# Performance work log

Hardware: AMD Instinct MI355X
Metric: run time of the kernel (lower is better)

## Reference

```python
import jax, jax.numpy as jnp
import numpy as np

B, CI, CO, H, W = 16, 256, 256, 64, 64
WDIM, NUM_FREQ, FREQ_DIM = 512, 16, 512
KS, PAD = 3, 1
SR = 64.0
LR_MULT = 1.0 / SR
GAIN = float(np.sqrt(1.0 / (CI * KS * KS)))
FREQ_GAIN = float(np.sqrt(1.0 / (FREQ_DIM * 2)))


def setup_inputs() -> dict:
    key = jax.random.key(0)
    ks = jax.random.split(key, 7)
    x = jax.random.normal(ks[0], (B, CI, H, W), dtype=jnp.float32)
    temb = jax.random.normal(ks[1], (B, WDIM), dtype=jnp.float32)
    basis = jax.random.normal(ks[2], (CI, KS, KS, FREQ_DIM), dtype=jnp.float32)
    magnitude = jax.random.normal(ks[3], (NUM_FREQ, CI, FREQ_DIM), dtype=jnp.float32)
    out_linear = jax.random.normal(ks[4], (CO, FREQ_DIM), dtype=jnp.float32)
    # FullyConnectedLayer init: weight = randn * (weight_init/lr_mult) = randn (both 1/SR)
    affine_w = jax.random.normal(ks[5], (NUM_FREQ, WDIM), dtype=jnp.float32)
    # bias param stores bias_init / lr_mult = 1 / (1/SR) = SR
    affine_b = jnp.full((NUM_FREQ,), SR, dtype=jnp.float32)
    conv_bias = jnp.zeros((CO,), dtype=jnp.float32)
    return {"x": x, "temb": temb, "basis": basis, "magnitude": magnitude,
            "out_linear": out_linear, "affine_w": affine_w, "affine_b": affine_b,
            "conv_bias": conv_bias}


def reference(x, temb, basis, magnitude, out_linear, affine_w, affine_b, conv_bias):
    # affine (FullyConnectedLayer, linear activation)
    w = affine_w * (LR_MULT / np.sqrt(WDIM))          # weight_gain
    s = temb @ w.T + affine_b * LR_MULT               # [B, K] per-sample freq weights
    # mix magnitude per sample: [K,I,F],[B,K] -> [B,I,F]
    mag_b = jnp.einsum('kif,bk->bif', magnitude, s) / np.sqrt(NUM_FREQ)
    # per-sample dynamic kernels: [I,h,w,F],[B,I,F],[O,F] -> [B,O,I,h,w]
    kernel = jnp.einsum('ihwf,bif,of->boihw', basis, mag_b, out_linear)
    kernel = kernel * (FREQ_GAIN * GAIN)
    kernel = kernel.reshape(B * CO, CI, KS, KS)
    # grouped conv, groups = batch
    xg = x.reshape(1, B * CI, H, W)
    y = jax.lax.conv_general_dilated(
        xg, kernel, window_strides=(1, 1), padding=[(PAD, PAD), (PAD, PAD)],
        dimension_numbers=('NCHW', 'OIHW', 'NCHW'), feature_group_count=B)
    y = y.reshape(B, CO, H, W)
    return jax.nn.silu(y) + conv_bias[None, :, None, None]
```

## Files before the change

kernel.cpp:

```cpp
#include <hip/hip_runtime.h>
#include <hip/hip_bf16.h>
#include <math.h>

#define B_    16
#define CI_   256
#define CO_   256
#define H_    64
#define W_    64
#define WDIM_ 512
#define NF_   16
#define FD_   512

typedef short bf16x8 __attribute__((ext_vector_type(8)));
typedef short s16x8  __attribute__((ext_vector_type(8)));
typedef float f32x4  __attribute__((ext_vector_type(4)));

__device__ __forceinline__ short f2bf(float f) {
  union { float f; unsigned u; } x; x.f = f;
  unsigned r = (x.u + 0x7FFFu + ((x.u >> 16) & 1u)) >> 16;
  return (short)r;
}
__device__ __forceinline__ float bf2f(short s) {
  union { unsigned u; float f; } x; x.u = ((unsigned)(unsigned short)s) << 16;
  return x.f;
}

__device__ __forceinline__ void gload16(const short* g, short* l) {
  __builtin_amdgcn_global_load_lds(
      (const __attribute__((address_space(1))) void*)g,
      (__attribute__((address_space(3))) void*)l, 16, 0, 0);
}

__device__ __forceinline__ size_t koff(int b, int kb, int cc, int t, int o) {
  return ((((((size_t)b * 4 + kb) * 8 + cc) * 9 + t) * 256) + o) * 8;
}
__device__ __forceinline__ size_t xoff(int b, int kb, int cc, int hp, int wp) {
  return ((((((size_t)b * 4 + kb) * 8 + cc) * 66 + hp) * 66) + wp) * 8;
}

__global__ __launch_bounds__(256) void prep_kernel(
    const float* __restrict__ temb, const float* __restrict__ affine_w,
    const float* __restrict__ affine_b, const float* __restrict__ out_linear,
    float* __restrict__ s_ws, short* __restrict__ olbf) {
  int tid = threadIdx.x;
  if (blockIdx.x == 0) {
    int b = tid >> 4, k = tid & 15;
    const float* t = temb + b * WDIM_;
    const float* w = affine_w + k * WDIM_;
    float acc = 0.f;
    for (int j = 0; j < WDIM_; j += 4) {
      float4 tv = *(const float4*)(t + j);
      float4 wv = *(const float4*)(w + j);
      acc += tv.x * wv.x + tv.y * wv.y + tv.z * wv.z + tv.w * wv.w;
    }
    const float WGAIN = 6.9053399e-4f;
    const float LRM   = 1.0f / 64.0f;
    s_ws[tid] = acc * WGAIN + affine_b[k] * LRM;
  } else {
    int e = (blockIdx.x - 1) * 256 + tid;
    const float* src = out_linear + (size_t)e * 8;
    s16x8 pk;
#pragma unroll
    for (int j = 0; j < 8; ++j) pk[j] = f2bf(src[j]);
    *(s16x8*)(olbf + (size_t)e * 8) = pk;
  }
}

__global__ __launch_bounds__(256) void magmix_kernel(
    const float* __restrict__ magnitude, const float* __restrict__ s_ws,
    short* __restrict__ mag_bf) {
  int bid = blockIdx.x;
  int i = bid >> 1;
  int f = ((bid & 1) << 8) + threadIdx.x;
  __shared__ float ssh[256];
  ssh[threadIdx.x] = s_ws[threadIdx.x];
  __syncthreads();
  float mg[16];
#pragma unroll
  for (int k = 0; k < 16; ++k)
    mg[k] = magnitude[(size_t)(k * CI_ + i) * FD_ + f];
#pragma unroll
  for (int b = 0; b < 16; ++b) {
    float acc = 0.f;
#pragma unroll
    for (int k = 0; k < 16; ++k) acc += mg[k] * ssh[b * 16 + k];
    mag_bf[(size_t)(b * CI_ + i) * FD_ + f] = f2bf(acc * 0.25f);
  }
}

__global__ __launch_bounds__(512) void synth_xpose_kernel(
    const float* __restrict__ basis, const short* __restrict__ mag_bf,
    const short* __restrict__ olbf, short* __restrict__ kbf,
    const float* __restrict__ x, short* __restrict__ xt) {
  __shared__ short smem_s[24576];
  int tid = threadIdx.x;

  if (blockIdx.x < 288) {
    short* alds = smem_s;
    short* blds = smem_s + 8192;
    int bid = blockIdx.x;
    int b  = bid / 18;
    int mt = bid - b * 18;
    int t   = mt >> 1;
    int i0g = (mt & 1) * 128;

    int lane = tid & 63;
    int wv = tid >> 6;
    int wm = wv >> 2, wn = wv & 3;
    int l15 = lane & 15, kb = lane >> 4;

    f32x4 acc[4][4];
#pragma unroll
    for (int m = 0; m < 4; ++m)
#pragma unroll
      for (int n = 0; n < 4; ++n) acc[m][n] = (f32x4)0.f;

    int ra = tid >> 2;
    int fsa = (tid & 3) * 16;
    int rb = tid >> 1;
    int fsb = (tid & 1) * 32;

    const float* bpA = basis + ((size_t)(i0g + ra) * 9 + t) * FD_ + fsa;
    const short* mpA = mag_bf + ((size_t)b * CI_ + i0g + ra) * FD_ + fsa;
    const short* opB = olbf + (size_t)rb * FD_ + fsb;

    for (int cc = 0; cc < 8; ++cc) {
      int f0 = cc * 64;
      __syncthreads();
#pragma unroll
      for (int u = 0; u < 2; ++u) {
        s16x8 m8 = *(const s16x8*)(mpA + f0 + u * 8);
        s16x8 pk;
#pragma unroll
        for (int j = 0; j < 2; ++j) {
          float4 b4 = *(const float4*)(bpA + f0 + u * 8 + j * 4);
          pk[j * 4 + 0] = f2bf(b4.x * bf2f(m8[j * 4 + 0]));
          pk[j * 4 + 1] = f2bf(b4.y * bf2f(m8[j * 4 + 1]));
          pk[j * 4 + 2] = f2bf(b4.z * bf2f(m8[j * 4 + 2]));
          pk[j * 4 + 3] = f2bf(b4.w * bf2f(m8[j * 4 + 3]));
        }
        int slot = (tid & 3) * 2 + u;
        *(s16x8*)&alds[ra * 64 + ((slot ^ (ra & 7)) << 3)] = pk;
      }
#pragma unroll
      for (int u = 0; u < 4; ++u) {
        s16x8 pk = *(const s16x8*)(opB + f0 + u * 8);
        int slot = (tid & 1) * 4 + u;
        *(s16x8*)&blds[rb * 64 + ((slot ^ (rb & 7)) << 3)] = pk;
      }
      __syncthreads();

#pragma unroll
      for (int ks = 0; ks < 2; ++ks) {
        bf16x8 afr[4], bfr[4];
#pragma unroll
        for (int m = 0; m < 4; ++m) {
          int row = wm * 64 + m * 16 + l15;
          int slot = ks * 4 + kb;
          afr[m] = *(const bf16x8*)&alds[row * 64 + ((slot ^ (row & 7)) << 3)];
        }
#pragma unroll
        for (int n = 0; n < 4; ++n) {
          int row = wn * 64 + n * 16 + l15;
          int slot = ks * 4 + kb;
          bfr[n] = *(const bf16x8*)&blds[row * 64 + ((slot ^ (row & 7)) << 3)];
        }
#pragma unroll
        for (int m = 0; m < 4; ++m)
#pragma unroll
          for (int n = 0; n < 4; ++n)
            acc[m][n] = __builtin_amdgcn_mfma_f32_16x16x32_bf16(afr[m], bfr[n], acc[m][n], 0, 0, 0);
      }
    }

    const float KSCALE = 1.0f / 1536.0f;
#pragma unroll
    for (int m = 0; m < 4; ++m) {
      int i_loc = i0g + wm * 64 + m * 16 + (lane >> 4) * 4;
      int kb2 = (i_loc >> 3) & 3;
      int cc2 = i_loc >> 5;
      int e2  = i_loc & 7;
#pragma unroll
      for (int n = 0; n < 4; ++n) {
        int o = wn * 64 + n * 16 + l15;
        short4 s4;
        s4.x = f2bf(acc[m][n][0] * KSCALE);
        s4.y = f2bf(acc[m][n][1] * KSCALE);
        s4.z = f2bf(acc[m][n][2] * KSCALE);
        s4.w = f2bf(acc[m][n][3] * KSCALE);
        *(short4*)(kbf + koff(b, kb2, cc2, t, o) + e2) = s4;
      }
    }
  } else {
    float* lx2 = (float*)smem_s;
    int bid = blockIdx.x - 288;
    int b = bid / 33, pr = bid - b * 33;
    int half = tid >> 8;
    int t2 = tid & 255;
    int hp = pr * 2 + half;
    bool interior = (hp >= 1 && hp <= 64);
    int h = hp - 1;
    const float* xb = x + ((size_t)b * CI_) * H_ * W_ + (size_t)h * W_;
    float* lx = lx2 + half * 2048;
    s16x8 z = (s16x8)0;
    int w = t2 >> 2, kb = t2 & 3;

    for (int cc = 0; cc < 8; ++cc) {
      __syncthreads();
      if (interior) {
        int rr = t2 >> 4, c4 = (t2 & 15) * 4;
        *(float4*)&lx[rr * 64 + c4] =
            *(const float4*)(xb + (size_t)(cc * 32 + rr) * H_ * W_ + c4);
        *(float4*)&lx[(rr + 16) * 64 + c4] =
            *(const float4*)(xb + (size_t)(cc * 32 + rr + 16) * H_ * W_ + c4);
      }
      __syncthreads();
      if (interior) {
        s16x8 o8;
#pragma unroll
        for (int k2 = 0; k2 < 8; ++k2) o8[k2] = f2bf(lx[(kb * 8 + k2) * 64 + w]);
        *(s16x8*)(xt + xoff(b, kb, cc, hp, w + 1)) = o8;
        if (w == 0) {
          *(s16x8*)(xt + xoff(b, kb, cc, hp, 0)) = z;
          *(s16x8*)(xt + xoff(b, kb, cc, hp, 65)) = z;
        }
      } else {
        for (int e = t2; e < 264; e += 256) {
          int kb2 = e / 66, wp = e - kb2 * 66;
          *(s16x8*)(xt + xoff(b, kb2, cc, hp, wp)) = z;
        }
      }
    }
  }
}

__global__ __launch_bounds__(256, 4) void conv_mfma_kernel(
    const short* __restrict__ xt, const short* __restrict__ kbf,
    const float* __restrict__ conv_bias, float* __restrict__ out) {
  int bid = ((blockIdx.x & 7) << 7) + (blockIdx.x >> 3);
  int b  = bid >> 6;
  int ot = (bid >> 4) & 3;
  int rt = bid & 15;
  int o_base = ot * 64;
  int r0 = rt * 4;
  int tid = threadIdx.x;
  int lane = tid & 63;
  int wv = tid >> 6;
  int orow = lane & 15, kb = lane >> 4;

  __shared__ short xs[25 * 512];

  f32x4 acc[4][4];
#pragma unroll
  for (int m = 0; m < 4; ++m)
#pragma unroll
    for (int n = 0; n < 4; ++n) acc[m][n] = (f32x4)0.f;

  const short* abase = kbf + koff(b, kb, 0, 0, o_base + orow);

  for (int cc = 0; cc < 8; ++cc) {
    __syncthreads();
    for (int ch = wv; ch < 25; ch += 4) {
      int D = ch * 1024 + lane * 16;
      int kb2 = D / 6400;
      int r = (D - kb2 * 6400) >> 4;
      r = r < 396 ? r : 395;
      int xr = (r * 1986) >> 17;
      int c = r - xr * 66;
      const short* src = xt + xoff(b, kb2, cc, r0 + xr, c);
      gload16(src, &xs[ch * 512]);
    }
    __syncthreads();

    const short* ac = abase + (size_t)cc * 18432;
#pragma unroll
    for (int t = 0; t < 9; ++t) {
      const int dh = t / 3 - 1, dw = t % 3 - 1;
      bf16x8 afr[4], bfr[4];
#pragma unroll
      for (int m = 0; m < 4; ++m)
        afr[m] = *(const bf16x8*)(ac + t * 2048 + m * 128);
      int xr = wv + 1 + dh;
#pragma unroll
      for (int n = 0; n < 4; ++n) {
        int xc = n * 16 + orow + 1 + dw;
        bfr[n] = *(const bf16x8*)&xs[(kb * 400 + xr * 66 + xc) * 8];
      }
#pragma unroll
      for (int m = 0; m < 4; ++m)
#pragma unroll
        for (int n = 0; n < 4; ++n)
          acc[m][n] = __builtin_amdgcn_mfma_f32_16x16x32_bf16(afr[m], bfr[n], acc[m][n], 0, 0, 0);
    }
  }

  int row = r0 + wv;
#pragma unroll
  for (int m = 0; m < 4; ++m) {
#pragma unroll
    for (int q = 0; q < 4; ++q) {
      int o = o_base + m * 16 + (lane >> 4) * 4 + q;
      float bias = conv_bias[o];
      size_t obase = (((size_t)b * CO_ + o) * H_ + row) * W_;
#pragma unroll
      for (int n = 0; n < 4; ++n) {
        float y = acc[m][n][q];
        out[obase + n * 16 + (lane & 15)] = y / (1.f + __expf(-y)) + bias;
      }
    }
  }
}

extern "C" void kernel_launch(void* const* d_in, const int* in_sizes, int n_in,
                              void* d_out, int out_size, void* d_ws, size_t ws_size,
                              hipStream_t stream) {
  const float* x          = (const float*)d_in[0];
  const float* temb       = (const float*)d_in[1];
  const float* basis      = (const float*)d_in[2];
  const float* magnitude  = (const float*)d_in[3];
  const float* out_linear = (const float*)d_in[4];
  const float* affine_w   = (const float*)d_in[5];
  const float* affine_b   = (const float*)d_in[6];
  const float* conv_bias  = (const float*)d_in[7];
  float* out = (float*)d_out;

  char* ws = (char*)d_ws;
  float* s_ws = (float*)ws;
  short* kbf  = (short*)(ws + 1024);
  short* xt   = (short*)(ws + 1024 + 18874368);
  short* mag_bf = (short*)(ws + 1024 + 18874368 + 35684352);
  short* olbf   = (short*)(ws + 1024 + 18874368 + 35684352 + 4194304);

  prep_kernel<<<65, 256, 0, stream>>>(temb, affine_w, affine_b, out_linear, s_ws, olbf);
  magmix_kernel<<<512, 256, 0, stream>>>(magnitude, s_ws, mag_bf);
  synth_xpose_kernel<<<816, 512, 0, stream>>>(basis, mag_bf, olbf, kbf, x, xt);
  conv_mfma_kernel<<<1024, 256, 0, stream>>>(xt, kbf, conv_bias, out);
}
```

Baseline: 136.2 us.

## Switch conv to 32x32x16 MFMA with 8-row tiles per block

The grouped-conv kernel now gives each block 8 output rows instead of 4 and uses 32x32x16 bf16 MFMA tiles instead of 16x16x32. This halves the grid and increases halo reuse, since 10 staged input rows serve 8 output rows rather than 6 serving 4. Global load addresses for the LDS staging are precomputed once. The cost is a larger LDS footprint, more accumulator registers, and launch bounds lowered to 2 blocks per SM, which reduces occupancy.

```diff
diff --git a/kernel.cpp b/kernel.cpp
--- a/kernel.cpp
+++ b/kernel.cpp
@@ -14,6 +14,7 @@
 typedef short bf16x8 __attribute__((ext_vector_type(8)));
 typedef short s16x8  __attribute__((ext_vector_type(8)));
 typedef float f32x4  __attribute__((ext_vector_type(4)));
+typedef float f32x16 __attribute__((ext_vector_type(16)));
 
 __device__ __forceinline__ short f2bf(float f) {
   union { float f; unsigned u; } x; x.f = f;
@@ -234,41 +235,51 @@
   }
 }
 
-__global__ __launch_bounds__(256, 4) void conv_mfma_kernel(
+__global__ __launch_bounds__(256, 2) void conv_mfma_kernel(
     const short* __restrict__ xt, const short* __restrict__ kbf,
     const float* __restrict__ conv_bias, float* __restrict__ out) {
-  int bid = ((blockIdx.x & 7) << 7) + (blockIdx.x >> 3);
-  int b  = bid >> 6;
-  int ot = (bid >> 4) & 3;
-  int rt = bid & 15;
+  int bid = ((blockIdx.x & 7) << 6) + (blockIdx.x >> 3);
+  int b  = bid >> 5;
+  int ot = (bid >> 3) & 3;
+  int rt = bid & 7;
   int o_base = ot * 64;
-  int r0 = rt * 4;
+  int r0 = rt * 8;
   int tid = threadIdx.x;
   int lane = tid & 63;
   int wv = tid >> 6;
-  int orow = lane & 15, kb = lane >> 4;
-
-  __shared__ short xs[25 * 512];
-
-  f32x4 acc[4][4];
-#pragma unroll
-  for (int m = 0; m < 4; ++m)
-#pragma unroll
-    for (int n = 0; n < 4; ++n) acc[m][n] = (f32x4)0.f;
-
-  const short* abase = kbf + koff(b, kb, 0, 0, o_base + orow);
+  int l31 = lane & 31;
+  int half = lane >> 5;
+
+  __shared__ short xs[42 * 512];
+
+  f32x16 acc[2][4];
+#pragma unroll
+  for (int m = 0; m < 2; ++m)
+#pragma unroll
+    for (int n = 0; n < 4; ++n) acc[m][n] = (f32x16)0.f;
+
+  const short* abase = kbf + koff(b, half, 0, 0, o_base + l31);
+
+  const short* xsrc[11];
+#pragma unroll
+  for (int j = 0; j < 11; ++j) {
+    int ch = wv + j * 4;
+    int s = ch * 64 + lane;
+    s = s < 2639 ? s : 2639;
+    int kb2 = s / 660;
+    int rem = s - kb2 * 660;
+    int r = rem / 66;
+    int c = rem - r * 66;
+    xsrc[j] = xt + xoff(b, kb2, 0, r0 + r, c);
+  }
 
   for (int cc = 0; cc < 8; ++cc) {
     __syncthreads();
-    for (int ch = wv; ch < 25; ch += 4) {
-      int D = ch * 1024 + lane * 16;
-      int kb2 = D / 6400;
-      int r = (D - kb2 * 6400) >> 4;
-      r = r < 396 ? r : 395;
-      int xr = (r * 1986) >> 17;
-      int c = r - xr * 66;
-      const short* src = xt + xoff(b, kb2, cc, r0 + xr, c);
-      gload16(src, &xs[ch * 512]);
+#pragma unroll
+    for (int j = 0; j < 11; ++j) {
+      int ch = wv + j * 4;
+      if (ch < 42)
+        gload16(xsrc[j] + (size_t)cc * 34848, &xs[ch * 512]);
     }
     __syncthreads();
 
@@ -276,36 +287,44 @@
 #pragma unroll
     for (int t = 0; t < 9; ++t) {
       const int dh = t / 3 - 1, dw = t % 3 - 1;
-      bf16x8 afr[4], bfr[4];
-#pragma unroll
-      for (int m = 0; m < 4; ++m)
-        afr[m] = *(const bf16x8*)(ac + t * 2048 + m * 128);
-      int xr = wv + 1 + dh;
-#pragma unroll
-      for (int n = 0; n < 4; ++n) {
-        int xc = n * 16 + orow + 1 + dw;
-        bfr[n] = *(const bf16x8*)&xs[(kb * 400 + xr * 66 + xc) * 8];
-      }
-#pragma unroll
-      for (int m = 0; m < 4; ++m)
-#pragma unroll
-        for (int n = 0; n < 4; ++n)
-          acc[m][n] = __builtin_amdgcn_mfma_f32_16x16x32_bf16(afr[m], bfr[n], acc[m][n], 0, 0, 0);
-    }
-  }
-
-  int row = r0 + wv;
-#pragma unroll
-  for (int m = 0; m < 4; ++m) {
-#pragma unroll
-    for (int q = 0; q < 4; ++q) {
-      int o = o_base + m * 16 + (lane >> 4) * 4 + q;
-      float bias = conv_bias[o];
-      size_t obase = (((size_t)b * CO_ + o) * H_ + row) * W_;
-#pragma unroll
-      for (int n = 0; n < 4; ++n) {
+      bf16x8 afr[2][2];
+#pragma unroll
+      for (int ks = 0; ks < 2; ++ks)
+#pragma unroll
+        for (int m = 0; m < 2; ++m)
+          afr[ks][m] = *(const bf16x8*)(ac + ks * 294912 + t * 2048 + m * 256);
+#pragma unroll
+      for (int ks = 0; ks < 2; ++ks) {
+        int kplane = ks * 2 + half;
+        bf16x8 bfr[4];
+#pragma unroll
+        for (int n = 0; n < 4; ++n) {
+          int rr = wv * 2 + (n >> 1) + dh + 1;
+          int xc = (n & 1) * 32 + l31 + dw + 1;
+          bfr[n] = *(const bf16x8*)&xs[(kplane * 660 + rr * 66 + xc) * 8];
+        }
+#pragma unroll
+        for (int m = 0; m < 2; ++m)
+#pragma unroll
+          for (int n = 0; n < 4; ++n)
+            acc[m][n] = __builtin_amdgcn_mfma_f32_32x32x16_bf16(afr[ks][m], bfr[n], acc[m][n], 0, 0, 0);
+      }
+    }
+  }
+
+#pragma unroll
+  for (int m = 0; m < 2; ++m) {
+#pragma unroll
+    for (int n = 0; n < 4; ++n) {
+      int row = r0 + wv * 2 + (n >> 1);
+      int colb = (n & 1) * 32;
+#pragma unroll
+      for (int q = 0; q < 16; ++q) {
+        int o = o_base + m * 32 + (q & 3) + 8 * (q >> 2) + 4 * half;
+        float bias = conv_bias[o];
         float y = acc[m][n][q];
-        out[obase + n * 16 + (lane & 15)] = y / (1.f + __expf(-y)) + bias;
+        out[(((size_t)b * CO_ + o) * H_ + row) * W_ + colb + l31] =
+            y / (1.f + __expf(-y)) + bias;
       }
     }
   }
@@ -334,5 +353,5 @@
   prep_kernel<<<65, 256, 0, stream>>>(temb, affine_w, affine_b, out_linear, s_ws, olbf);
   magmix_kernel<<<512, 256, 0, stream>>>(magnitude, s_ws, mag_bf);
   synth_xpose_kernel<<<816, 512, 0, stream>>>(basis, mag_bf, olbf, kbf, x, xt);
-  conv_mfma_kernel<<<1024, 256, 0, stream>>>(xt, kbf, conv_bias, out);
-}
+  conv_mfma_kernel<<<512, 256, 0, stream>>>(xt, kbf, conv_bias, out);
+}
```

Result: slower. 183.9 us (+35.0%).

## Fuse prep and magmix kernels; stage two channel chunks per conv barrier

Applied to the files above, without the earlier changes.

The affine projection is merged into the magnitude-mixing kernel. Each block recomputes the 16x16 frequency weights into shared memory, which removes a kernel launch and a global round trip. The conv kernel now loads two 32-channel chunks into a doubled LDS buffer per barrier pair and precomputes the source pointers, which halves the number of sync/load phases. Occupancy is lowered to 3 blocks per CU to fit the larger LDS tile. Each mixing block now redundantly recomputes the small affine GEMV.

```diff
diff --git a/kernel.cpp b/kernel.cpp
--- a/kernel.cpp
+++ b/kernel.cpp
@@ -38,12 +38,27 @@
   return ((((((size_t)b * 4 + kb) * 8 + cc) * 66 + hp) * 66) + wp) * 8;
 }
 
-__global__ __launch_bounds__(256) void prep_kernel(
-    const float* __restrict__ temb, const float* __restrict__ affine_w,
-    const float* __restrict__ affine_b, const float* __restrict__ out_linear,
-    float* __restrict__ s_ws, short* __restrict__ olbf) {
+__global__ __launch_bounds__(256) void head_kernel(
+    const float* __restrict__ magnitude, const float* __restrict__ temb,
+    const float* __restrict__ affine_w, const float* __restrict__ affine_b,
+    const float* __restrict__ out_linear,
+    short* __restrict__ mag_bf, short* __restrict__ olbf) {
   int tid = threadIdx.x;
-  if (blockIdx.x == 0) {
+  if (blockIdx.x >= 512) {
+    int base = (blockIdx.x - 512) * 512 + tid;
+#pragma unroll
+    for (int r = 0; r < 2; ++r) {
+      int e = base + r * 256;
+      const float* src = out_linear + (size_t)e * 8;
+      s16x8 pk;
+#pragma unroll
+      for (int j = 0; j < 8; ++j) pk[j] = f2bf(src[j]);
+      *(s16x8*)(olbf + (size_t)e * 8) = pk;
+    }
+    return;
+  }
+  __shared__ float ssh[256];
+  {
     int b = tid >> 4, k = tid & 15;
     const float* t = temb + b * WDIM_;
     const float* w = affine_w + k * WDIM_;
@@ -55,26 +70,11 @@
     }
     const float WGAIN = 6.9053399e-4f;
     const float LRM   = 1.0f / 64.0f;
-    s_ws[tid] = acc * WGAIN + affine_b[k] * LRM;
-  } else {
-    int e = (blockIdx.x - 1) * 256 + tid;
-    const float* src = out_linear + (size_t)e * 8;
-    s16x8 pk;
-#pragma unroll
-    for (int j = 0; j < 8; ++j) pk[j] = f2bf(src[j]);
-    *(s16x8*)(olbf + (size_t)e * 8) = pk;
-  }
-}
-
-__global__ __launch_bounds__(256) void magmix_kernel(
-    const float* __restrict__ magnitude, const float* __restrict__ s_ws,
-    short* __restrict__ mag_bf) {
-  int bid = blockIdx.x;
-  int i = bid >> 1;
-  int f = ((bid & 1) << 8) + threadIdx.x;
-  __shared__ float ssh[256];
-  ssh[threadIdx.x] = s_ws[threadIdx.x];
+    ssh[tid] = acc * WGAIN + affine_b[k] * LRM;
+  }
   __syncthreads();
+  int i = blockIdx.x >> 1;
+  int f = ((blockIdx.x & 1) << 8) + tid;
   float mg[16];
 #pragma unroll
   for (int k = 0; k < 16; ++k)
@@ -234,7 +234,7 @@
   }
 }
 
-__global__ __launch_bounds__(256, 4) void conv_mfma_kernel(
+__global__ __launch_bounds__(256, 3) void conv_mfma_kernel(
     const short* __restrict__ xt, const short* __restrict__ kbf,
     const float* __restrict__ conv_bias, float* __restrict__ out) {
   int bid = ((blockIdx.x & 7) << 7) + (blockIdx.x >> 3);
@@ -248,7 +248,7 @@
   int wv = tid >> 6;
   int orow = lane & 15, kb = lane >> 4;
 
-  __shared__ short xs[25 * 512];
+  __shared__ short xs[50 * 512];
 
   f32x4 acc[4][4];
 #pragma unroll
@@ -258,39 +258,53 @@
 
   const short* abase = kbf + koff(b, kb, 0, 0, o_base + orow);
 
-  for (int cc = 0; cc < 8; ++cc) {
+  const short* xsrc[13];
+#pragma unroll
+  for (int j = 0; j < 13; ++j) {
+    int ch = wv + j * 4;
+    ch = ch < 50 ? ch : 49;
+    int sub = ch >= 25 ? 1 : 0;
+    int D = (ch - sub * 25) * 1024 + lane * 16;
+    int kb2 = D / 6400;
+    int r = (D - kb2 * 6400) >> 4;
+    r = r < 396 ? r : 395;
+    int xr = (r * 1986) >> 17;
+    int c = r - xr * 66;
+    xsrc[j] = xt + xoff(b, kb2, sub, r0 + xr, c);
+  }
+
+  for (int c4 = 0; c4 < 4; ++c4) {
     __syncthreads();
-    for (int ch = wv; ch < 25; ch += 4) {
-      int D = ch * 1024 + lane * 16;
-      int kb2 = D / 6400;
-      int r = (D - kb2 * 6400) >> 4;
-      r = r < 396 ? r : 395;
-      int xr = (r * 1986) >> 17;
-      int c = r - xr * 66;
-      const short* src = xt + xoff(b, kb2, cc, r0 + xr, c);
-      gload16(src, &xs[ch * 512]);
+#pragma unroll
+    for (int j = 0; j < 13; ++j) {
+      int ch = wv + j * 4;
+      if (ch < 50)
+        gload16(xsrc[j] + (size_t)c4 * 69696, &xs[ch * 512]);
     }
     __syncthreads();
 
-    const short* ac = abase + (size_t)cc * 18432;
-#pragma unroll
-    for (int t = 0; t < 9; ++t) {
-      const int dh = t / 3 - 1, dw = t % 3 - 1;
-      bf16x8 afr[4], bfr[4];
-#pragma unroll
-      for (int m = 0; m < 4; ++m)
-        afr[m] = *(const bf16x8*)(ac + t * 2048 + m * 128);
-      int xr = wv + 1 + dh;
-#pragma unroll
-      for (int n = 0; n < 4; ++n) {
-        int xc = n * 16 + orow + 1 + dw;
-        bfr[n] = *(const bf16x8*)&xs[(kb * 400 + xr * 66 + xc) * 8];
-      }
-#pragma unroll
-      for (int m = 0; m < 4; ++m)
-#pragma unroll
-        for (int n = 0; n < 4; ++n)
-          acc[m][n] = __builtin_amdgcn_mfma_f32_16x16x32_bf16(afr[m], bfr[n], acc[m][n], 0, 0, 0);
+#pragma unroll
+    for (int sub = 0; sub < 2; ++sub) {
+      const short* ac = abase + (size_t)(c4 * 2 + sub) * 18432;
+#pragma unroll
+      for (int t = 0; t < 9; ++t) {
+        const int dh = t / 3 - 1, dw = t % 3 - 1;
+        bf16x8 afr[4], bfr[4];
+#pragma unroll
+        for (int m = 0; m < 4; ++m)
+          afr[m] = *(const bf16x8*)(ac + t * 2048 + m * 128);
+        int xr = wv + 1 + dh;
+#pragma unroll
+        for (int n = 0; n < 4; ++n) {
+          int xc = n * 16 + orow + 1 + dw;
+          bfr[n] = *(const bf16x8*)&xs[sub * 12800 + (kb * 400 + xr * 66 + xc) * 8];
+        }
+#pragma unroll
+        for (int m = 0; m < 4; ++m)
+#pragma unroll
+          for (int n = 0; n < 4; ++n)
+            acc[m][n] = __builtin_amdgcn_mfma_f32_16x16x32_bf16(afr[m], bfr[n], acc[m][n], 0, 0, 0);
+      }
     }
   }
 
@@ -325,14 +339,13 @@
   float* out = (float*)d_out;
 
   char* ws = (char*)d_ws;
-  float* s_ws = (float*)ws;
   short* kbf  = (short*)(ws + 1024);
   short* xt   = (short*)(ws + 1024 + 18874368);
   short* mag_bf = (short*)(ws + 1024 + 18874368 + 35684352);
   short* olbf   = (short*)(ws + 1024 + 18874368 + 35684352 + 4194304);
 
-  prep_kernel<<<65, 256, 0, stream>>>(temb, affine_w, affine_b, out_linear, s_ws, olbf);
-  magmix_kernel<<<512, 256, 0, stream>>>(magnitude, s_ws, mag_bf);
+  head_kernel<<<576, 256, 0, stream>>>(magnitude, temb, affine_w, affine_b,
+                                       out_linear, mag_bf, olbf);
   synth_xpose_kernel<<<816, 512, 0, stream>>>(basis, mag_bf, olbf, kbf, x, xt);
   conv_mfma_kernel<<<1024, 256, 0, stream>>>(xt, kbf, conv_bias, out);
 }
```

Result: slower. 179.0 us (+31.4%).
